# Kernel optimization log

Measured on AMD Instinct MI355X. Metric: run time of the kernel, lower is better.

## Reference

```python
import jax, jax.numpy as jnp
import numpy as np

H = 16
D = 64
EPS = 1e-6

def _phi(x):
    # elu_feature_map: elu(x) + 1
    return jax.nn.elu(x) + 1.0

def setup_inputs() -> dict:
    key = jax.random.key(0)
    k1, k2, k3, k4 = jax.random.split(key, 4)
    B, N = 4, 4096
    query = jax.random.normal(k1, (B, N, H * D), dtype=jnp.float32)
    key_t = jax.random.normal(k2, (B, N, H * D), dtype=jnp.float32)
    value = jax.random.normal(k3, (B, N, H * D), dtype=jnp.float32)
    W_out = jax.random.normal(k4, (D, H * D), dtype=jnp.float32) * (1.0 / np.sqrt(H * D))
    b_out = jnp.zeros((D,), dtype=jnp.float32)
    return {"query": query, "key": key_t, "value": value, "W_out": W_out, "b_out": b_out}

def reference(query, key, value, W_out, b_out):
    B, N, _ = query.shape
    # b n (h d) -> b h n d
    def split_heads(x):
        return x.reshape(B, N, H, D).transpose(0, 2, 1, 3)
    q = split_heads(query)
    k = split_heads(key)
    v = split_heads(value)
    Q = _phi(q)  # [B,H,N,D]
    K = _phi(k)
    # KV aggregation: O(N D^2)
    KV = jnp.einsum('bhnd,bhnm->bhdm', K, v)          # [B,H,D,D]
    Ksum = K.sum(axis=2)                               # [B,H,D]
    Z = 1.0 / (jnp.einsum('bhnd,bhd->bhn', Q, Ksum) + EPS)  # [B,H,N]
    out = jnp.einsum('bhnd,bhdm,bhn->bhnm', Q, KV, Z)  # [B,H,N,D]
    # b h n d -> b n h d -> (b*n, h*d)
    out = out.transpose(0, 2, 1, 3).reshape(B * N, H * D)
    return out @ W_out.T + b_out
```

## Files before the change

### kernel.cpp

```cpp
#include <hip/hip_runtime.h>

#define B_  4
#define N_  4096
#define H_  16
#define BH_ 64
#define S_  16
#define HS_ 4
#define ST_ 72
#define EPS_ 1e-6f

#define NST_ 40
#define TSH_ 2584
#define BUFH_ (8 * TSH_)

typedef _Float16 h2  __attribute__((ext_vector_type(2)));
typedef _Float16 h8  __attribute__((ext_vector_type(8)));
typedef float    f4v __attribute__((ext_vector_type(4)));

struct H2x2 { h2 a, b; };
struct H2x4 { h2 e[4]; };

__device__ __forceinline__ h8 ld_h8(const _Float16* p) {
    f4v r = *(const f4v*)p;
    return __builtin_bit_cast(h8, r);
}
__device__ __forceinline__ H2x4 ld_h2x4(const _Float16* p) {
    f4v r = *(const f4v*)p;
    return __builtin_bit_cast(H2x4, r);
}
__device__ __forceinline__ void st_h2x2(_Float16* p, h2 a, h2 b) {
    H2x2 t{a, b};
    *(float2*)p = __builtin_bit_cast(float2, t);
}
__device__ __forceinline__ float phi(float x) {
    return x > 0.0f ? x + 1.0f : __expf(x);
}
__device__ __forceinline__ float fdot2(h2 a, h2 b, float c) {
    return __builtin_amdgcn_fdot2(a, b, c, false);
}
__device__ __forceinline__ f4v gload(const void* p) {
    f4v r;
    asm volatile("global_load_dwordx4 %0, %1, off"
                 : "=v"(r) : "v"(p) : "memory");
    return r;
}
#define VMW(N)                                                    \
    do {                                                          \
        asm volatile("s_waitcnt vmcnt(" #N ")" ::: "memory");     \
        __builtin_amdgcn_sched_barrier(0);                        \
    } while (0)

__device__ __forceinline__ void barrier_lgkm() {
    asm volatile("s_waitcnt lgkmcnt(0)" ::: "memory");
    __builtin_amdgcn_sched_barrier(0);
    __builtin_amdgcn_s_barrier();
}

__global__ __launch_bounds__(512, 2) void k_kvpart(const float* __restrict__ K,
                                                   const float* __restrict__ V,
                                                   float* __restrict__ kvpart,
                                                   float* __restrict__ kspart) {
    const int s = blockIdx.x, hq = blockIdx.y, b = blockIdx.z;
    const int t = threadIdx.x, wv = t >> 6, lane = t & 63;
    const int hp = lane >> 4;
    const int l15 = lane & 15;

    __shared__ __align__(16) _Float16 pool[2 * BUFH_];

    f4v kA[4], vA[4], kB[4], vB[4];

    auto LOADX = [&](f4v* kreg, f4v* vreg, int chunk) {
        const int n0 = s * 256 + chunk * 32 + 4 * wv;
        const size_t fo0 = (size_t)(b * N_ + n0) * 1024 + hq * 256 + lane * 4;
        const float* gk = K + fo0;
        const float* gv = V + fo0;
        kreg[0] = gload(gk);        kreg[1] = gload(gk + 1024);
        kreg[2] = gload(gk + 2048); kreg[3] = gload(gk + 3072);
        vreg[0] = gload(gv);        vreg[1] = gload(gv + 1024);
        vreg[2] = gload(gv + 2048); vreg[3] = gload(gv + 3072);
    };
    auto STOREX = [&](const f4v* kreg, const f4v* vreg, int buf) {
        _Float16* Kt = pool + buf * BUFH_ + (hp * 2) * TSH_;
        _Float16* Vt = Kt + TSH_;
        const int nn = 4 * wv;
#pragma unroll
        for (int dj = 0; dj < 4; ++dj) {
            int d = 4 * l15 + dj;
            h2 lo, hi;
            lo.x = (_Float16)phi(kreg[0][dj]); lo.y = (_Float16)phi(kreg[1][dj]);
            hi.x = (_Float16)phi(kreg[2][dj]); hi.y = (_Float16)phi(kreg[3][dj]);
            st_h2x2(&Kt[d * NST_ + nn], lo, hi);
            lo.x = (_Float16)vreg[0][dj]; lo.y = (_Float16)vreg[1][dj];
            hi.x = (_Float16)vreg[2][dj]; hi.y = (_Float16)vreg[3][dj];
            st_h2x2(&Vt[d * NST_ + nn], lo, hi);
        }
    };

    const int hh = wv >> 1, dhalf = wv & 1;
    const int rA = l15;
    const int fo = (lane >> 4) * 8;

    f4v acc[2][4];
#pragma unroll
    for (int a = 0; a < 2; ++a)
#pragma unroll
        for (int m = 0; m < 4; ++m) acc[a][m] = (f4v){0.f, 0.f, 0.f, 0.f};
    f4v accK[2];
    accK[0] = (f4v){0.f, 0.f, 0.f, 0.f};
    accK[1] = (f4v){0.f, 0.f, 0.f, 0.f};
    h8 ones;
#pragma unroll
    for (int i = 0; i < 8; ++i) ones[i] = (_Float16)1.0f;

    auto COMPUTE = [&](int buf) {
        const _Float16* Kt = pool + buf * BUFH_ + (hh * 2) * TSH_;
        const _Float16* Vt = Kt + TSH_;
        h8 a0 = ld_h8(&Kt[(32 * dhalf + rA) * NST_ + fo]);
        h8 a1 = ld_h8(&Kt[(32 * dhalf + 16 + rA) * NST_ + fo]);
        h8 b0 = ld_h8(&Vt[(rA) * NST_ + fo]);
        h8 b1 = ld_h8(&Vt[(16 + rA) * NST_ + fo]);
        h8 b2 = ld_h8(&Vt[(32 + rA) * NST_ + fo]);
        h8 b3 = ld_h8(&Vt[(48 + rA) * NST_ + fo]);
        acc[0][0] = __builtin_amdgcn_mfma_f32_16x16x32_f16(a0, b0, acc[0][0], 0, 0, 0);
        acc[0][1] = __builtin_amdgcn_mfma_f32_16x16x32_f16(a0, b1, acc[0][1], 0, 0, 0);
        acc[0][2] = __builtin_amdgcn_mfma_f32_16x16x32_f16(a0, b2, acc[0][2], 0, 0, 0);
        acc[0][3] = __builtin_amdgcn_mfma_f32_16x16x32_f16(a0, b3, acc[0][3], 0, 0, 0);
        acc[1][0] = __builtin_amdgcn_mfma_f32_16x16x32_f16(a1, b0, acc[1][0], 0, 0, 0);
        acc[1][1] = __builtin_amdgcn_mfma_f32_16x16x32_f16(a1, b1, acc[1][1], 0, 0, 0);
        acc[1][2] = __builtin_amdgcn_mfma_f32_16x16x32_f16(a1, b2, acc[1][2], 0, 0, 0);
        acc[1][3] = __builtin_amdgcn_mfma_f32_16x16x32_f16(a1, b3, acc[1][3], 0, 0, 0);
        accK[0]   = __builtin_amdgcn_mfma_f32_16x16x32_f16(a0, ones, accK[0], 0, 0, 0);
        accK[1]   = __builtin_amdgcn_mfma_f32_16x16x32_f16(a1, ones, accK[1], 0, 0, 0);
    };

    LOADX(kA, vA, 0);
    LOADX(kB, vB, 1);
    VMW(8);  STOREX(kA, vA, 0); barrier_lgkm();
    LOADX(kA, vA, 2); COMPUTE(0); VMW(8); STOREX(kB, vB, 1); barrier_lgkm();
    LOADX(kB, vB, 3); COMPUTE(1); VMW(8); STOREX(kA, vA, 0); barrier_lgkm();
    LOADX(kA, vA, 4); COMPUTE(0); VMW(8); STOREX(kB, vB, 1); barrier_lgkm();
    LOADX(kB, vB, 5); COMPUTE(1); VMW(8); STOREX(kA, vA, 0); barrier_lgkm();
    LOADX(kA, vA, 6); COMPUTE(0); VMW(8); STOREX(kB, vB, 1); barrier_lgkm();
    LOADX(kB, vB, 7); COMPUTE(1); VMW(8); STOREX(kA, vA, 0); barrier_lgkm();
    COMPUTE(0); VMW(0); STOREX(kB, vB, 1); barrier_lgkm();
    COMPUTE(1);

    const int bh = b * 16 + hq * 4 + hh;
    float* outp = kvpart + (size_t)(bh * S_ + s) * 4096;
#pragma unroll
    for (int a = 0; a < 2; ++a)
#pragma unroll
        for (int m = 0; m < 4; ++m)
#pragma unroll
            for (int r = 0; r < 4; ++r) {
                int d = 32 * dhalf + 16 * a + hp * 4 + r;
                int mm = 16 * m + l15;
                outp[d * 64 + mm] = acc[a][m][r];
            }
    if (l15 == 0) {
        float* ksp = kspart + (size_t)(bh * S_ + s) * 64;
#pragma unroll
        for (int a = 0; a < 2; ++a)
#pragma unroll
            for (int r = 0; r < 4; ++r) {
                int d = 32 * dhalf + 16 * a + hp * 4 + r;
                ksp[d] = accK[a][r];
            }
    }
}

__global__ __launch_bounds__(256, 2) void k_makeM(const float* __restrict__ kvpart,
                                                  const float* __restrict__ kspart,
                                                  const float* __restrict__ W,
                                                  _Float16* __restrict__ Mt,
                                                  float* __restrict__ Ksum) {
    const int bh = blockIdx.x, dq = blockIdx.y;
    const int h  = bh & 15;
    const int t  = threadIdx.x;

    __shared__ float KVs[16][68];
    __shared__ float Ws[64][68];

    const f4v* W4  = (const f4v*)W;

    f4v rr[S_];
    {
        const int row = t >> 4, c4 = t & 15;
        const float* g = kvpart + ((size_t)(bh * S_) * 4096 +
                                   (dq * 16 + row) * 64 + c4 * 4);
#pragma unroll
        for (int s = 0; s < S_; ++s) rr[s] = gload(g + (size_t)s * 4096);
    }
    for (int idx = t; idx < 1024; idx += 256) {
        int wrow = idx >> 4, wc = idx & 15;
        *(f4v*)&Ws[wrow][wc * 4] = W4[(size_t)wrow * 256 + h * 16 + wc];
    }
    if (dq == 0 && t < 64) {
        float ks = 0.f;
#pragma unroll
        for (int s = 0; s < S_; ++s) ks += kspart[(size_t)(bh * S_ + s) * 64 + t];
        Ksum[(size_t)bh * 64 + t] = ks;
    }
    VMW(0);
    {
        const int row = t >> 4, c4 = t & 15;
        f4v r = {0.f, 0.f, 0.f, 0.f};
#pragma unroll
        for (int s = 0; s < S_; ++s) r += rr[s];
        *(f4v*)&KVs[row][c4 * 4] = r;
    }
    __syncthreads();

    const int j = t >> 2, dl = (t & 3) * 4;
    float acc[4] = {0.f, 0.f, 0.f, 0.f};
#pragma unroll 4
    for (int m4 = 0; m4 < 16; ++m4) {
        f4v wr  = *(const f4v*)&Ws[j][m4 * 4];
        f4v kv0 = *(const f4v*)&KVs[dl + 0][m4 * 4];
        f4v kv1 = *(const f4v*)&KVs[dl + 1][m4 * 4];
        f4v kv2 = *(const f4v*)&KVs[dl + 2][m4 * 4];
        f4v kv3 = *(const f4v*)&KVs[dl + 3][m4 * 4];
        acc[0] += wr[0] * kv0[0] + wr[1] * kv0[1] + wr[2] * kv0[2] + wr[3] * kv0[3];
        acc[1] += wr[0] * kv1[0] + wr[1] * kv1[1] + wr[2] * kv1[2] + wr[3] * kv1[3];
        acc[2] += wr[0] * kv2[0] + wr[1] * kv2[1] + wr[2] * kv2[2] + wr[3] * kv2[3];
        acc[3] += wr[0] * kv3[0] + wr[1] * kv3[1] + wr[2] * kv3[2] + wr[3] * kv3[3];
    }
    h2 lo, hi;
    lo.x = (_Float16)acc[0]; lo.y = (_Float16)acc[1];
    hi.x = (_Float16)acc[2]; hi.y = (_Float16)acc[3];
    H2x2 pk{lo, hi};
    *(float2*)&Mt[((size_t)bh * 64 + j) * 64 + dq * 16 + dl] =
        __builtin_bit_cast(float2, pk);
}

__global__ __launch_bounds__(256, 2) void k_out(const float* __restrict__ Q,
                                                const _Float16* __restrict__ Mtg,
                                                const float* __restrict__ Ksum,
                                                float* __restrict__ outpart) {
    const int nc = blockIdx.x, b = blockIdx.y, hs = blockIdx.z;
    const int n0 = nc * 64;
    const int t = threadIdx.x, w = t >> 6, lane = t & 63;
    const int rp4 = t >> 4, c4 = t & 15;

    __shared__ __align__(16) _Float16 pool[2 * 2 * 64 * ST_];
    __shared__ float zz[64];
    __shared__ h2 Kss[2][32];

    f4v qr[4], mr[2];
    float ksa = 0.f, ksb = 0.f;
    auto LOAD = [&](int hh) {
        const int h = hs * 4 + hh, bh = b * 16 + h;
        const float* gq = Q + ((size_t)(b * N_ + n0 + rp4) * 1024 + h * 64 + c4 * 4);
        qr[0] = gload(gq);
        qr[1] = gload(gq + 16 * 1024);
        qr[2] = gload(gq + 32 * 1024);
        qr[3] = gload(gq + 48 * 1024);
        const _Float16* gm = Mtg + ((size_t)bh * 4096 + t * 8);
        mr[0] = gload(gm);
        mr[1] = gload(gm + 2048);
        if (t < 32) {
            ksa = Ksum[(size_t)bh * 64 + 2 * t];
            ksb = Ksum[(size_t)bh * 64 + 2 * t + 1];
        }
    };
    auto STORE = [&](int buf) {
        _Float16* Qp = pool + buf * (2 * 64 * ST_);
        _Float16* Mt = Qp + 64 * ST_;
#pragma unroll
        for (int r = 0; r < 4; ++r) {
            int row = rp4 + 16 * r;
            h2 p0, p1;
            p0.x = (_Float16)phi(qr[r][0]); p0.y = (_Float16)phi(qr[r][1]);
            p1.x = (_Float16)phi(qr[r][2]); p1.y = (_Float16)phi(qr[r][3]);
            st_h2x2(&Qp[row * ST_ + 4 * c4], p0, p1);
        }
        *(f4v*)&Mt[(t >> 3) * ST_ + (t & 7) * 8] = mr[0];
        *(f4v*)&Mt[((t + 256) >> 3) * ST_ + (t & 7) * 8] = mr[1];
        if (t < 32) { h2 kk; kk.x = (_Float16)ksa; kk.y = (_Float16)ksb; Kss[buf][t] = kk; }
    };

    const int tn0 = 2 * (w >> 1), tj0 = 2 * (w & 1);
    const int rA = lane & 15, fo = (lane >> 4) * 8;
    float facc[2][2][4] = {{{0.f}}};

    LOAD(0);
    VMW(0);
    STORE(0);

    for (int hh = 0; hh < 4; ++hh) {
        if (hh + 1 < 4) LOAD(hh + 1);
        barrier_lgkm();
        const int buf = hh & 1;
        const _Float16* Qp = pool + buf * (2 * 64 * ST_);
        const _Float16* Mt = Qp + 64 * ST_;

        if (t < 64) {
            float zp = 0.f;
#pragma unroll
            for (int c = 0; c < 8; ++c) {
                H2x4 x = ld_h2x4(&Qp[t * ST_ + c * 8]);
#pragma unroll
                for (int i = 0; i < 4; ++i) zp = fdot2(x.e[i], Kss[buf][c * 4 + i], zp);
            }
            zz[t] = 1.0f / (zp + EPS_);
        }
        barrier_lgkm();

        f4v acc[2][2];
#pragma unroll
        for (int a = 0; a < 2; ++a)
#pragma unroll
            for (int bb = 0; bb < 2; ++bb) acc[a][bb] = (f4v){0.f, 0.f, 0.f, 0.f};
#pragma unroll
        for (int ks = 0; ks < 2; ++ks) {
            h8 a0 = ld_h8(&Qp[(16 * (tn0 + 0) + rA) * ST_ + ks * 32 + fo]);
            h8 a1 = ld_h8(&Qp[(16 * (tn0 + 1) + rA) * ST_ + ks * 32 + fo]);
            h8 b0 = ld_h8(&Mt[(16 * (tj0 + 0) + rA) * ST_ + ks * 32 + fo]);
            h8 b1 = ld_h8(&Mt[(16 * (tj0 + 1) + rA) * ST_ + ks * 32 + fo]);
            acc[0][0] = __builtin_amdgcn_mfma_f32_16x16x32_f16(a0, b0, acc[0][0], 0, 0, 0);
            acc[0][1] = __builtin_amdgcn_mfma_f32_16x16x32_f16(a0, b1, acc[0][1], 0, 0, 0);
            acc[1][0] = __builtin_amdgcn_mfma_f32_16x16x32_f16(a1, b0, acc[1][0], 0, 0, 0);
            acc[1][1] = __builtin_amdgcn_mfma_f32_16x16x32_f16(a1, b1, acc[1][1], 0, 0, 0);
        }
#pragma unroll
        for (int a = 0; a < 2; ++a)
#pragma unroll
            for (int r = 0; r < 4; ++r) {
                int row = 16 * (tn0 + a) + (lane >> 4) * 4 + r;
                float z = zz[row];
                facc[a][0][r] += z * acc[a][0][r];
                facc[a][1][r] += z * acc[a][1][r];
            }
        if (hh + 1 < 4) {
            VMW(0);
            STORE((hh + 1) & 1);
        }
    }

    float* op = outpart + (size_t)hs * (B_ * N_ * 64);
#pragma unroll
    for (int a = 0; a < 2; ++a)
#pragma unroll
        for (int bb = 0; bb < 2; ++bb)
#pragma unroll
            for (int r = 0; r < 4; ++r) {
                int n = 16 * (tn0 + a) + (lane >> 4) * 4 + r;
                int j = 16 * (tj0 + bb) + (lane & 15);
                op[(size_t)(b * N_ + n0 + n) * 64 + j] = facc[a][bb][r];
            }
}

__global__ __launch_bounds__(256, 4) void k_red(const float* __restrict__ outpart,
                                                const float* __restrict__ bout,
                                                float* __restrict__ out) {
    const int p = blockIdx.x * 256 + threadIdx.x;
    const f4v* P4 = (const f4v*)outpart;
    const f4v* B4 = (const f4v*)bout;
    f4v o = B4[p & 15];
    const int stride = B_ * N_ * 64 / 4;
    f4v pr[HS_];
#pragma unroll
    for (int hs = 0; hs < HS_; ++hs) pr[hs] = P4[(size_t)hs * stride + p];
#pragma unroll
    for (int hs = 0; hs < HS_; ++hs) o += pr[hs];
    ((f4v*)out)[p] = o;
}

extern "C" void kernel_launch(void* const* d_in, const int* in_sizes, int n_in,
                              void* d_out, int out_size, void* d_ws, size_t ws_size,
                              hipStream_t stream) {
    const float* q  = (const float*)d_in[0];
    const float* k  = (const float*)d_in[1];
    const float* v  = (const float*)d_in[2];
    const float* W  = (const float*)d_in[3];
    const float* bo = (const float*)d_in[4];
    float* out = (float*)d_out;

    float* ws      = (float*)d_ws;
    float* kvpart  = ws;
    float* kspart  = kvpart + (size_t)BH_ * S_ * 4096;
    float* Mt      = kspart + (size_t)BH_ * S_ * 64;
    float* Ksum    = Mt + (size_t)BH_ * 4096 / 2;
    float* outpart = Ksum + (size_t)BH_ * 64;

    k_kvpart<<<dim3(S_, 4, 4), 512, 0, stream>>>(k, v, kvpart, kspart);
    k_makeM<<<dim3(BH_, 4), 256, 0, stream>>>(kvpart, kspart, W, (_Float16*)Mt, Ksum);
    k_out<<<dim3(N_ / 64, B_, HS_), 256, 0, stream>>>(q, (const _Float16*)Mt, Ksum, outpart);
    k_red<<<B_ * N_ * 64 / 4 / 256, 256, 0, stream>>>(outpart, bo, out);
}
```

Before: 222.5 us.

## Fuse head-split reduction into output kernel and make KV partials wave-private

The output kernel now loops over all 16 heads in one block and adds the bias in its epilogue. This removes the separate reduction kernel and the write and re-read of four partial output buffers. The KV-partial kernel is reorganised so each wave owns one head with a private LDS tile, which removes the block-wide barriers. The K column sum is now taken with fdot2 over LDS instead of extra MFMAs against a ones vector. In exchange the output kernel launches four times fewer blocks, each doing a longer serial head loop, so there is less parallelism to hide latency.

```diff
diff --git a/kernel.cpp b/kernel.cpp
--- a/kernel.cpp
+++ b/kernel.cpp
@@ -5,13 +5,12 @@
 #define H_  16
 #define BH_ 64
 #define S_  16
-#define HS_ 4
 #define ST_ 72
 #define EPS_ 1e-6f
 
 #define NST_ 40
-#define TSH_ 2584
-#define BUFH_ (8 * TSH_)
+#define WTILE_ (64 * NST_)
+#define WPOOL_ (2 * WTILE_)
 
 typedef _Float16 h2  __attribute__((ext_vector_type(2)));
 typedef _Float16 h8  __attribute__((ext_vector_type(8)));
@@ -50,123 +49,110 @@
         __builtin_amdgcn_sched_barrier(0);                        \
     } while (0)
 
-__device__ __forceinline__ void barrier_lgkm() {
-    asm volatile("s_waitcnt lgkmcnt(0)" ::: "memory");
-    __builtin_amdgcn_sched_barrier(0);
-    __builtin_amdgcn_s_barrier();
-}
-
-__global__ __launch_bounds__(512, 2) void k_kvpart(const float* __restrict__ K,
+__global__ __launch_bounds__(256, 2) void k_kvpart(const float* __restrict__ K,
                                                    const float* __restrict__ V,
                                                    float* __restrict__ kvpart,
                                                    float* __restrict__ kspart) {
-    const int s = blockIdx.x, hq = blockIdx.y, b = blockIdx.z;
+    const int s = blockIdx.x, h4 = blockIdx.y, b = blockIdx.z;
     const int t = threadIdx.x, wv = t >> 6, lane = t & 63;
-    const int hp = lane >> 4;
-    const int l15 = lane & 15;
-
-    __shared__ __align__(16) _Float16 pool[2 * BUFH_];
-
-    f4v kA[4], vA[4], kB[4], vB[4];
-
-    auto LOADX = [&](f4v* kreg, f4v* vreg, int chunk) {
-        const int n0 = s * 256 + chunk * 32 + 4 * wv;
-        const size_t fo0 = (size_t)(b * N_ + n0) * 1024 + hq * 256 + lane * 4;
-        const float* gk = K + fo0;
-        const float* gv = V + fo0;
-        kreg[0] = gload(gk);        kreg[1] = gload(gk + 1024);
-        kreg[2] = gload(gk + 2048); kreg[3] = gload(gk + 3072);
-        vreg[0] = gload(gv);        vreg[1] = gload(gv + 1024);
-        vreg[2] = gload(gv + 2048); vreg[3] = gload(gv + 3072);
-    };
-    auto STOREX = [&](const f4v* kreg, const f4v* vreg, int buf) {
-        _Float16* Kt = pool + buf * BUFH_ + (hp * 2) * TSH_;
-        _Float16* Vt = Kt + TSH_;
-        const int nn = 4 * wv;
+    const int rp = lane >> 4, c4 = lane & 15;
+    const int h = h4 * 4 + wv;
+
+    __shared__ __align__(16) _Float16 pool[4 * WPOOL_];
+
+    _Float16* Kt = pool + wv * WPOOL_;
+    _Float16* Vt = Kt + WTILE_;
+
+    f4v kr[8], vr[8];
+    const float* baseK = K + ((size_t)(b * N_ + s * 256) * 1024 + h * 64 + c4 * 4);
+    const float* baseV = V + ((size_t)(b * N_ + s * 256) * 1024 + h * 64 + c4 * 4);
+
+    auto LOADX = [&](int chunk) {
+        const int ro = (chunk * 32 + 8 * rp) * 1024;
+        const float* gk = baseK + ro;
+        const float* gv = baseV + ro;
+#pragma unroll
+        for (int r = 0; r < 8; ++r) kr[r] = gload(gk + r * 1024);
+#pragma unroll
+        for (int r = 0; r < 8; ++r) vr[r] = gload(gv + r * 1024);
+    };
+    auto STOREX = [&]() {
+        const int nn = 8 * rp;
 #pragma unroll
         for (int dj = 0; dj < 4; ++dj) {
-            int d = 4 * l15 + dj;
+            const int d = 4 * c4 + dj;
             h2 lo, hi;
-            lo.x = (_Float16)phi(kreg[0][dj]); lo.y = (_Float16)phi(kreg[1][dj]);
-            hi.x = (_Float16)phi(kreg[2][dj]); hi.y = (_Float16)phi(kreg[3][dj]);
+            lo.x = (_Float16)phi(kr[0][dj]); lo.y = (_Float16)phi(kr[1][dj]);
+            hi.x = (_Float16)phi(kr[2][dj]); hi.y = (_Float16)phi(kr[3][dj]);
             st_h2x2(&Kt[d * NST_ + nn], lo, hi);
-            lo.x = (_Float16)vreg[0][dj]; lo.y = (_Float16)vreg[1][dj];
-            hi.x = (_Float16)vreg[2][dj]; hi.y = (_Float16)vreg[3][dj];
+            lo.x = (_Float16)phi(kr[4][dj]); lo.y = (_Float16)phi(kr[5][dj]);
+            hi.x = (_Float16)phi(kr[6][dj]); hi.y = (_Float16)phi(kr[7][dj]);
+            st_h2x2(&Kt[d * NST_ + nn + 4], lo, hi);
+            lo.x = (_Float16)vr[0][dj]; lo.y = (_Float16)vr[1][dj];
+            hi.x = (_Float16)vr[2][dj]; hi.y = (_Float16)vr[3][dj];
             st_h2x2(&Vt[d * NST_ + nn], lo, hi);
-        }
-    };
-
-    const int hh = wv >> 1, dhalf = wv & 1;
-    const int rA = l15;
-    const int fo = (lane >> 4) * 8;
-
-    f4v acc[2][4];
-#pragma unroll
-    for (int a = 0; a < 2; ++a)
-#pragma unroll
-        for (int m = 0; m < 4; ++m) acc[a][m] = (f4v){0.f, 0.f, 0.f, 0.f};
-    f4v accK[2];
-    accK[0] = (f4v){0.f, 0.f, 0.f, 0.f};
-    accK[1] = (f4v){0.f, 0.f, 0.f, 0.f};
-    h8 ones;
-#pragma unroll
-    for (int i = 0; i < 8; ++i) ones[i] = (_Float16)1.0f;
-
-    auto COMPUTE = [&](int buf) {
-        const _Float16* Kt = pool + buf * BUFH_ + (hh * 2) * TSH_;
-        const _Float16* Vt = Kt + TSH_;
-        h8 a0 = ld_h8(&Kt[(32 * dhalf + rA) * NST_ + fo]);
-        h8 a1 = ld_h8(&Kt[(32 * dhalf + 16 + rA) * NST_ + fo]);
-        h8 b0 = ld_h8(&Vt[(rA) * NST_ + fo]);
-        h8 b1 = ld_h8(&Vt[(16 + rA) * NST_ + fo]);
-        h8 b2 = ld_h8(&Vt[(32 + rA) * NST_ + fo]);
-        h8 b3 = ld_h8(&Vt[(48 + rA) * NST_ + fo]);
-        acc[0][0] = __builtin_amdgcn_mfma_f32_16x16x32_f16(a0, b0, acc[0][0], 0, 0, 0);
-        acc[0][1] = __builtin_amdgcn_mfma_f32_16x16x32_f16(a0, b1, acc[0][1], 0, 0, 0);
-        acc[0][2] = __builtin_amdgcn_mfma_f32_16x16x32_f16(a0, b2, acc[0][2], 0, 0, 0);
-        acc[0][3] = __builtin_amdgcn_mfma_f32_16x16x32_f16(a0, b3, acc[0][3], 0, 0, 0);
-        acc[1][0] = __builtin_amdgcn_mfma_f32_16x16x32_f16(a1, b0, acc[1][0], 0, 0, 0);
-        acc[1][1] = __builtin_amdgcn_mfma_f32_16x16x32_f16(a1, b1, acc[1][1], 0, 0, 0);
-        acc[1][2] = __builtin_amdgcn_mfma_f32_16x16x32_f16(a1, b2, acc[1][2], 0, 0, 0);
-        acc[1][3] = __builtin_amdgcn_mfma_f32_16x16x32_f16(a1, b3, acc[1][3], 0, 0, 0);
-        accK[0]   = __builtin_amdgcn_mfma_f32_16x16x32_f16(a0, ones, accK[0], 0, 0, 0);
-        accK[1]   = __builtin_amdgcn_mfma_f32_16x16x32_f16(a1, ones, accK[1], 0, 0, 0);
-    };
-
-    LOADX(kA, vA, 0);
-    LOADX(kB, vB, 1);
-    VMW(8);  STOREX(kA, vA, 0); barrier_lgkm();
-    LOADX(kA, vA, 2); COMPUTE(0); VMW(8); STOREX(kB, vB, 1); barrier_lgkm();
-    LOADX(kB, vB, 3); COMPUTE(1); VMW(8); STOREX(kA, vA, 0); barrier_lgkm();
-    LOADX(kA, vA, 4); COMPUTE(0); VMW(8); STOREX(kB, vB, 1); barrier_lgkm();
-    LOADX(kB, vB, 5); COMPUTE(1); VMW(8); STOREX(kA, vA, 0); barrier_lgkm();
-    LOADX(kA, vA, 6); COMPUTE(0); VMW(8); STOREX(kB, vB, 1); barrier_lgkm();
-    LOADX(kB, vB, 7); COMPUTE(1); VMW(8); STOREX(kA, vA, 0); barrier_lgkm();
-    COMPUTE(0); VMW(0); STOREX(kB, vB, 1); barrier_lgkm();
-    COMPUTE(1);
-
-    const int bh = b * 16 + hq * 4 + hh;
+            lo.x = (_Float16)vr[4][dj]; lo.y = (_Float16)vr[5][dj];
+            hi.x = (_Float16)vr[6][dj]; hi.y = (_Float16)vr[7][dj];
+            st_h2x2(&Vt[d * NST_ + nn + 4], lo, hi);
+        }
+    };
+
+    f4v acc[4][4];
+#pragma unroll
+    for (int i = 0; i < 4; ++i)
+#pragma unroll
+        for (int j = 0; j < 4; ++j) acc[i][j] = (f4v){0.f, 0.f, 0.f, 0.f};
+    float ksum = 0.f;
+    h2 one2; one2.x = (_Float16)1.0f; one2.y = (_Float16)1.0f;
+
+    const int fo = rp * 8;
+
+    auto COMPUTE = [&]() {
+        h8 af[4], bf[4];
+#pragma unroll
+        for (int i = 0; i < 4; ++i) {
+            af[i] = ld_h8(&Kt[(16 * i + c4) * NST_ + fo]);
+            bf[i] = ld_h8(&Vt[(16 * i + c4) * NST_ + fo]);
+        }
+#pragma unroll
+        for (int i = 0; i < 4; ++i)
+#pragma unroll
+            for (int j = 0; j < 4; ++j)
+                acc[i][j] = __builtin_amdgcn_mfma_f32_16x16x32_f16(af[i], bf[j], acc[i][j], 0, 0, 0);
+#pragma unroll
+        for (int q = 0; q < 4; ++q) {
+            H2x4 x = ld_h2x4(&Kt[lane * NST_ + q * 8]);
+#pragma unroll
+            for (int i = 0; i < 4; ++i) ksum = fdot2(x.e[i], one2, ksum);
+        }
+    };
+
+    LOADX(0);
+    VMW(0);
+    STOREX();
+#pragma unroll
+    for (int c = 0; c < 8; ++c) {
+        if (c < 7) LOADX(c + 1);
+        COMPUTE();
+        if (c < 7) {
+            VMW(0);
+            STOREX();
+        }
+    }
+
+    const int bh = b * 16 + h;
     float* outp = kvpart + (size_t)(bh * S_ + s) * 4096;
 #pragma unroll
-    for (int a = 0; a < 2; ++a)
-#pragma unroll
-        for (int m = 0; m < 4; ++m)
+    for (int i = 0; i < 4; ++i)
+#pragma unroll
+        for (int j = 0; j < 4; ++j)
 #pragma unroll
             for (int r = 0; r < 4; ++r) {
-                int d = 32 * dhalf + 16 * a + hp * 4 + r;
-                int mm = 16 * m + l15;
-                outp[d * 64 + mm] = acc[a][m][r];
+                const int d = 16 * i + rp * 4 + r;
+                const int m = 16 * j + c4;
+                outp[d * 64 + m] = acc[i][j][r];
             }
-    if (l15 == 0) {
-        float* ksp = kspart + (size_t)(bh * S_ + s) * 64;
-#pragma unroll
-        for (int a = 0; a < 2; ++a)
-#pragma unroll
-            for (int r = 0; r < 4; ++r) {
-                int d = 32 * dhalf + 16 * a + hp * 4 + r;
-                ksp[d] = accK[a][r];
-            }
-    }
+    kspart[(size_t)(bh * S_ + s) * 64 + lane] = ksum;
 }
 
 __global__ __launch_bounds__(256, 2) void k_makeM(const float* __restrict__ kvpart,
@@ -236,8 +222,9 @@
 __global__ __launch_bounds__(256, 2) void k_out(const float* __restrict__ Q,
                                                 const _Float16* __restrict__ Mtg,
                                                 const float* __restrict__ Ksum,
-                                                float* __restrict__ outpart) {
-    const int nc = blockIdx.x, b = blockIdx.y, hs = blockIdx.z;
+                                                const float* __restrict__ bout,
+                                                float* __restrict__ out) {
+    const int nc = blockIdx.x, b = blockIdx.y;
     const int n0 = nc * 64;
     const int t = threadIdx.x, w = t >> 6, lane = t & 63;
     const int rp4 = t >> 4, c4 = t & 15;
@@ -249,8 +236,8 @@
     f4v qr[4], mr[2];
     float ksa = 0.f, ksb = 0.f;
     auto LOAD = [&](int hh) {
-        const int h = hs * 4 + hh, bh = b * 16 + h;
-        const float* gq = Q + ((size_t)(b * N_ + n0 + rp4) * 1024 + h * 64 + c4 * 4);
+        const int bh = b * 16 + hh;
+        const float* gq = Q + ((size_t)(b * N_ + n0 + rp4) * 1024 + hh * 64 + c4 * 4);
         qr[0] = gload(gq);
         qr[1] = gload(gq + 16 * 1024);
         qr[2] = gload(gq + 32 * 1024);
@@ -287,9 +274,9 @@
     VMW(0);
     STORE(0);
 
-    for (int hh = 0; hh < 4; ++hh) {
-        if (hh + 1 < 4) LOAD(hh + 1);
-        barrier_lgkm();
+    for (int hh = 0; hh < 16; ++hh) {
+        if (hh + 1 < 16) LOAD(hh + 1);
+        __syncthreads();
         const int buf = hh & 1;
         const _Float16* Qp = pool + buf * (2 * 64 * ST_);
         const _Float16* Mt = Qp + 64 * ST_;
@@ -304,7 +291,7 @@
             }
             zz[t] = 1.0f / (zp + EPS_);
         }
-        barrier_lgkm();
+        __syncthreads();
 
         f4v acc[2][2];
 #pragma unroll
@@ -331,39 +318,24 @@
                 facc[a][0][r] += z * acc[a][0][r];
                 facc[a][1][r] += z * acc[a][1][r];
             }
-        if (hh + 1 < 4) {
+        if (hh + 1 < 16) {
             VMW(0);
             STORE((hh + 1) & 1);
         }
     }
 
-    float* op = outpart + (size_t)hs * (B_ * N_ * 64);
 #pragma unroll
     for (int a = 0; a < 2; ++a)
 #pragma unroll
-        for (int bb = 0; bb < 2; ++bb)
+        for (int bb = 0; bb < 2; ++bb) {
+            const int j = 16 * (tj0 + bb) + (lane & 15);
+            const float bj = bout[j];
 #pragma unroll
             for (int r = 0; r < 4; ++r) {
                 int n = 16 * (tn0 + a) + (lane >> 4) * 4 + r;
-                int j = 16 * (tj0 + bb) + (lane & 15);
-                op[(size_t)(b * N_ + n0 + n) * 64 + j] = facc[a][bb][r];
+                out[(size_t)(b * N_ + n0 + n) * 64 + j] = bj + facc[a][bb][r];
             }
-}
-
-__global__ __launch_bounds__(256, 4) void k_red(const float* __restrict__ outpart,
-                                                const float* __restrict__ bout,
-                                                float* __restrict__ out) {
-    const int p = blockIdx.x * 256 + threadIdx.x;
-    const f4v* P4 = (const f4v*)outpart;
-    const f4v* B4 = (const f4v*)bout;
-    f4v o = B4[p & 15];
-    const int stride = B_ * N_ * 64 / 4;
-    f4v pr[HS_];
-#pragma unroll
-    for (int hs = 0; hs < HS_; ++hs) pr[hs] = P4[(size_t)hs * stride + p];
-#pragma unroll
-    for (int hs = 0; hs < HS_; ++hs) o += pr[hs];
-    ((f4v*)out)[p] = o;
+        }
 }
 
 extern "C" void kernel_launch(void* const* d_in, const int* in_sizes, int n_in,
@@ -381,10 +353,8 @@
     float* kspart  = kvpart + (size_t)BH_ * S_ * 4096;
     float* Mt      = kspart + (size_t)BH_ * S_ * 64;
     float* Ksum    = Mt + (size_t)BH_ * 4096 / 2;
-    float* outpart = Ksum + (size_t)BH_ * 64;
-
-    k_kvpart<<<dim3(S_, 4, 4), 512, 0, stream>>>(k, v, kvpart, kspart);
+
+    k_kvpart<<<dim3(S_, 4, 4), 256, 0, stream>>>(k, v, kvpart, kspart);
     k_makeM<<<dim3(BH_, 4), 256, 0, stream>>>(kvpart, kspart, W, (_Float16*)Mt, Ksum);
-    k_out<<<dim3(N_ / 64, B_, HS_), 256, 0, stream>>>(q, (const _Float16*)Mt, Ksum, outpart);
-    k_red<<<B_ * N_ * 64 / 4 / 256, 256, 0, stream>>>(outpart, bo, out);
-}
+    k_out<<<dim3(N_ / 64, B_), 256, 0, stream>>>(q, (const _Float16*)Mt, Ksum, bo, out);
+}
```

New measurement: 226.7 us. No clear change (+1.9%).
